# Kernel optimization log

Measured on AMD Instinct MI355X. Metric: run time of the kernel, lower is better.

The kernel has to match this reference:

```python
import jax, jax.numpy as jnp
import numpy as np

HEAD_NUM = 16
ROPE_BASE = 10000.0


def _rotate_half(x):
    # interleaved pairs: (x0,x1,x2,x3,...) -> (-x1,x0,-x3,x2,...)
    x_even = x[..., ::2]
    x_odd = x[..., 1::2]
    return jnp.stack((-x_odd, x_even), axis=-1).reshape(x.shape)


def _rope_cos_sin(seq_len, head_dim):
    half = head_dim // 2
    inv_freq = 1.0 / (ROPE_BASE ** (jnp.arange(half, dtype=jnp.float32) / half))
    t = jnp.arange(seq_len, dtype=jnp.float32)
    freqs = t[:, None] * inv_freq[None, :]            # [S, half]
    cos = jnp.repeat(jnp.cos(freqs), 2, axis=-1)       # [S, D]
    sin = jnp.repeat(jnp.sin(freqs), 2, axis=-1)       # [S, D]
    return cos, sin


def setup_inputs() -> dict:
    key = jax.random.key(0)
    ks = jax.random.split(key, 9)
    B, S, H = 2, 2048, 2048
    std = 1.0 / np.sqrt(H)
    return {
        "x": jax.random.normal(ks[0], (B, S, H), jnp.float32),
        "Wq": jax.random.normal(ks[1], (H, H), jnp.float32) * std,
        "bq": jax.random.normal(ks[2], (H,), jnp.float32) * std,
        "Wk": jax.random.normal(ks[3], (H, H), jnp.float32) * std,
        "bk": jax.random.normal(ks[4], (H,), jnp.float32) * std,
        "Wv": jax.random.normal(ks[5], (H, H), jnp.float32) * std,
        "bv": jax.random.normal(ks[6], (H,), jnp.float32) * std,
        "Wo": jax.random.normal(ks[7], (H, H), jnp.float32) * std,
        "bo": jax.random.normal(ks[8], (H,), jnp.float32) * std,
    }


def reference(x, Wq, bq, Wk, bk, Wv, bv, Wo, bo):
    B, S, H = x.shape
    nh = HEAD_NUM
    d = H // nh
    scale = jnp.float32(np.sqrt(d))

    def proj(W, b):
        y = x @ W.T + b                                 # torch Linear: x W^T + b
        return y.reshape(B, S, nh, d).transpose(0, 2, 1, 3)  # [B, nh, S, d]

    Q = proj(Wq, bq)
    K = proj(Wk, bk)
    V = proj(Wv, bv)

    cos, sin = _rope_cos_sin(S, d)                      # [S, d]
    Q = Q * cos + _rotate_half(Q) * sin
    K = K * cos + _rotate_half(K) * sin

    scores = jnp.einsum("bhqd,bhkd->bhqk", Q, K) / scale  # [B, nh, S, S]
    causal = jnp.tril(jnp.ones((S, S), dtype=bool))
    scores = jnp.where(causal, scores, jnp.float32(-jnp.inf))
    attn = jax.nn.softmax(scores, axis=-1)
    out = jnp.einsum("bhqk,bhkd->bhqd", attn, V)        # [B, nh, S, d]
    out = out.transpose(0, 2, 1, 3).reshape(B, S, H)
    return out @ Wo.T + bo
```

## Files before the change

### kernel.cpp

```cpp
#include <hip/hip_runtime.h>
#include <math.h>

typedef __bf16 bf16x8 __attribute__((ext_vector_type(8)));
typedef float floatx4 __attribute__((ext_vector_type(4)));

__device__ __forceinline__ unsigned short f32_to_bf16(float f) {
  unsigned int u = __float_as_uint(f);
  u = u + 0x7FFFu + ((u >> 16) & 1u);
  return (unsigned short)(u >> 16);
}
__device__ __forceinline__ float bf16_to_f32(unsigned short s) {
  return __uint_as_float(((unsigned int)s) << 16);
}

__device__ __forceinline__ void gld_lds16(const unsigned short* g,
                                          unsigned short* l) {
  __builtin_amdgcn_global_load_lds(
      (const __attribute__((address_space(1))) unsigned int*)g,
      (__attribute__((address_space(3))) unsigned int*)l, 16, 0, 0);
}

__global__ void cast_kernel(const float* __restrict__ in,
                            unsigned short* __restrict__ out, int n4) {
  int i = blockIdx.x * blockDim.x + threadIdx.x;
  if (i >= n4) return;
  const float4 v = reinterpret_cast<const float4*>(in)[i];
  ushort4 o;
  o.x = f32_to_bf16(v.x); o.y = f32_to_bf16(v.y);
  o.z = f32_to_bf16(v.z); o.w = f32_to_bf16(v.w);
  reinterpret_cast<ushort4*>(out)[i] = o;
}

__global__ void rope_table_kernel(float2* __restrict__ tab, int total) {
  int idx = blockIdx.x * blockDim.x + threadIdx.x;
  if (idx >= total) return;
  const int s = idx >> 6, i = idx & 63;
  const float inv = powf(10000.0f, -(float)i * (1.0f / 64.0f));
  const float ang = (float)s * inv;
  tab[idx] = make_float2(cosf(ang), sinf(ang));
}

template <int EPI>
__global__ __launch_bounds__(256) void gemm_fused(
    const unsigned short* __restrict__ A, const unsigned short* __restrict__ B,
    const float* __restrict__ bias, float* __restrict__ Cf,
    unsigned short* __restrict__ Cb, const float2* __restrict__ tab,
    float scl, int M, int N, int K, int S) {
  __shared__ unsigned short As[128 * 64];
  __shared__ unsigned short Bs[128 * 64];
  const int t = threadIdx.x;
  const int lane = t & 63;
  const int w = t >> 6;
  const int bm = blockIdx.y * 128;
  const int bn = blockIdx.x * 128;
  const int wm = (w & 1) * 64;
  const int wn = (w >> 1) * 64;
  const int m16 = lane & 15;
  const int quad = lane >> 4;
  const int key = m16 & 7;

  const int lr = lane >> 3;
  const int lc = ((lane & 7) ^ lr) * 8;

  floatx4 acc[4][4];
#pragma unroll
  for (int i = 0; i < 4; ++i)
#pragma unroll
    for (int j = 0; j < 4; ++j) acc[i][j] = floatx4{0.f, 0.f, 0.f, 0.f};

  const unsigned short* Abase = A + (size_t)(bm + w * 32 + lr) * K + lc;
  const unsigned short* Bbase = B + (size_t)(bn + w * 32 + lr) * K + lc;

  for (int k0 = 0; k0 < K; k0 += 64) {
    __syncthreads();
#pragma unroll
    for (int it = 0; it < 4; ++it) {
      gld_lds16(Abase + (size_t)it * 8 * K + k0, &As[(w * 4 + it) * 512]);
      gld_lds16(Bbase + (size_t)it * 8 * K + k0, &Bs[(w * 4 + it) * 512]);
    }
    __syncthreads();
#pragma unroll
    for (int ks = 0; ks < 64; ks += 32) {
      const int ck = ks >> 3;
      bf16x8 af[4], bfr[4];
#pragma unroll
      for (int i = 0; i < 4; ++i)
        af[i] = *reinterpret_cast<const bf16x8*>(
            &As[(wm + i * 16 + m16) * 64 + ((ck | quad) ^ key) * 8]);
#pragma unroll
      for (int j = 0; j < 4; ++j)
        bfr[j] = *reinterpret_cast<const bf16x8*>(
            &Bs[(wn + j * 16 + m16) * 64 + ((ck | quad) ^ key) * 8]);
#pragma unroll
      for (int i = 0; i < 4; ++i)
#pragma unroll
        for (int j = 0; j < 4; ++j)
          acc[i][j] = __builtin_amdgcn_mfma_f32_16x16x32_bf16(
              af[i], bfr[j], acc[i][j], 0, 0, 0);
    }
  }

#pragma unroll
  for (int i = 0; i < 4; ++i) {
    const int rbase = bm + wm + i * 16 + quad * 4;
#pragma unroll
    for (int j = 0; j < 4; ++j) {
      const int col = bn + wn + j * 16 + m16;
      const float bv = bias[col];
      if (EPI == 0) {
#pragma unroll
        for (int r = 0; r < 4; ++r)
          Cf[(size_t)(rbase + r) * N + col] = acc[i][j][r] + bv;
      } else if (EPI == 1) {
        const int pi = (col & 127) >> 1;
#pragma unroll
        for (int r = 0; r < 4; ++r) {
          const int row = rbase + r;
          const int s = row & (S - 1);
          const float v = acc[i][j][r] + bv;
          const float vp = __shfl_xor(v, 1);
          const float2 cs = tab[s * 64 + pi];
          const float oe = (v * cs.x - vp * cs.y) * scl;
          const float oo = (vp * cs.x + v * cs.y) * scl;
          if ((m16 & 1) == 0) {
            const unsigned pk =
                (unsigned)f32_to_bf16(oe) | ((unsigned)f32_to_bf16(oo) << 16);
            *reinterpret_cast<unsigned*>(Cb + (size_t)row * N + col) = pk;
          }
        }
      } else {
        const int b = rbase >> 11;
        const int s = rbase & (S - 1);
        ushort4 pk;
        pk.x = f32_to_bf16(acc[i][j][0] + bv);
        pk.y = f32_to_bf16(acc[i][j][1] + bv);
        pk.z = f32_to_bf16(acc[i][j][2] + bv);
        pk.w = f32_to_bf16(acc[i][j][3] + bv);
        *reinterpret_cast<ushort4*>(
            Cb + ((size_t)((b << 11) + col)) * S + s) = pk;
      }
    }
  }
}

constexpr int F_BQ = 128, F_BK = 64, F_DH = 128;
constexpr int KS_STR = 136;
constexpr int VS_STR = 72;
constexpr int PS_STR = 72;

__global__ __launch_bounds__(256, 2) void fattn_kernel(
    const unsigned short* __restrict__ Qb, const unsigned short* __restrict__ Kb,
    const unsigned short* __restrict__ Vtb, unsigned short* __restrict__ Ob,
    int S, int H, int nh) {
  __shared__ unsigned short Ks[F_BK * KS_STR];
  __shared__ unsigned short Vts[F_DH * VS_STR];
  __shared__ unsigned short Ps[F_BQ * PS_STR];

  const int t = threadIdx.x;
  const int lane = t & 63;
  const int w = t >> 6;
  const int l15 = lane & 15;
  const int quad = lane >> 4;

  const int i = blockIdx.x;
  const int bh = i & 31;
  const int qt = (i < 256) ? (i >> 5) : (15 - ((i - 256) >> 5));
  const int h = bh & 15;
  const int b = bh >> 4;
  const int q0 = qt * F_BQ;

  const unsigned short* Qrow = Qb + ((size_t)(b * S + q0)) * H + h * F_DH;
  const unsigned short* Krow = Kb + ((size_t)b * S) * H + h * F_DH;
  const unsigned short* Vtrow = Vtb + ((size_t)bh * F_DH) * S;
  unsigned short* Orow = Ob + ((size_t)(b * S + q0)) * H + h * F_DH;

  bf16x8 aq[2][4];
#pragma unroll
  for (int qg = 0; qg < 2; ++qg)
#pragma unroll
    for (int ks = 0; ks < 4; ++ks)
      aq[qg][ks] = *reinterpret_cast<const bf16x8*>(
          Qrow + (size_t)(w * 32 + qg * 16 + l15) * H + ks * 32 + quad * 8);

  floatx4 oacc[2][8];
#pragma unroll
  for (int qg = 0; qg < 2; ++qg)
#pragma unroll
    for (int dj = 0; dj < 8; ++dj) oacc[qg][dj] = floatx4{0.f, 0.f, 0.f, 0.f};
  float lpart[2][4] = {{0.f, 0.f, 0.f, 0.f}, {0.f, 0.f, 0.f, 0.f}};
  int qrow[2][4];
#pragma unroll
  for (int qg = 0; qg < 2; ++qg)
#pragma unroll
    for (int r = 0; r < 4; ++r)
      qrow[qg][r] = q0 + w * 32 + qg * 16 + quad * 4 + r;

  const int ntile = q0 / F_BK + 2;
  for (int tile = 0; tile < ntile; ++tile) {
    const int k0 = tile * F_BK;
    __syncthreads();
    {
      const int kt = t >> 2, c0 = (t & 3) * 32;
      const unsigned short* g = Krow + (size_t)(k0 + kt) * H + c0;
#pragma unroll
      for (int ii = 0; ii < 4; ++ii)
        *reinterpret_cast<uint4*>(&Ks[kt * KS_STR + c0 + ii * 8]) =
            *reinterpret_cast<const uint4*>(g + ii * 8);
    }
    {
      const int d = t >> 1, c0 = (t & 1) * 32;
      const unsigned short* g = Vtrow + (size_t)d * S + k0 + c0;
#pragma unroll
      for (int ii = 0; ii < 4; ++ii)
        *reinterpret_cast<uint4*>(&Vts[d * VS_STR + c0 + ii * 8]) =
            *reinterpret_cast<const uint4*>(g + ii * 8);
    }
    __syncthreads();

    floatx4 sacc[2][4];
#pragma unroll
    for (int qg = 0; qg < 2; ++qg)
#pragma unroll
      for (int j = 0; j < 4; ++j) sacc[qg][j] = floatx4{0.f, 0.f, 0.f, 0.f};
#pragma unroll
    for (int j = 0; j < 4; ++j) {
      bf16x8 bk[4];
#pragma unroll
      for (int ks = 0; ks < 4; ++ks)
        bk[ks] = *reinterpret_cast<const bf16x8*>(
            &Ks[(j * 16 + l15) * KS_STR + ks * 32 + quad * 8]);
#pragma unroll
      for (int qg = 0; qg < 2; ++qg)
#pragma unroll
        for (int ks = 0; ks < 4; ++ks)
          sacc[qg][j] = __builtin_amdgcn_mfma_f32_16x16x32_bf16(
              aq[qg][ks], bk[ks], sacc[qg][j], 0, 0, 0);
    }

#pragma unroll
    for (int qg = 0; qg < 2; ++qg)
#pragma unroll
      for (int j = 0; j < 4; ++j) {
        const int ktg = k0 + j * 16 + l15;
#pragma unroll
        for (int r = 0; r < 4; ++r) {
          const float p =
              (ktg <= qrow[qg][r]) ? exp2f(sacc[qg][j][r]) : 0.0f;
          lpart[qg][r] += p;
          Ps[(w * 32 + qg * 16 + quad * 4 + r) * PS_STR + j * 16 + l15] =
              f32_to_bf16(p);
        }
      }

#pragma unroll
    for (int ks2 = 0; ks2 < 2; ++ks2) {
      bf16x8 ap[2];
#pragma unroll
      for (int qg = 0; qg < 2; ++qg)
        ap[qg] = *reinterpret_cast<const bf16x8*>(
            &Ps[(w * 32 + qg * 16 + l15) * PS_STR + ks2 * 32 + quad * 8]);
#pragma unroll
      for (int dj = 0; dj < 8; ++dj) {
        const bf16x8 bv = *reinterpret_cast<const bf16x8*>(
            &Vts[(dj * 16 + l15) * VS_STR + ks2 * 32 + quad * 8]);
#pragma unroll
        for (int qg = 0; qg < 2; ++qg)
          oacc[qg][dj] = __builtin_amdgcn_mfma_f32_16x16x32_bf16(
              ap[qg], bv, oacc[qg][dj], 0, 0, 0);
      }
    }
  }

#pragma unroll
  for (int qg = 0; qg < 2; ++qg)
#pragma unroll
    for (int r = 0; r < 4; ++r) {
      float l = lpart[qg][r];
      l += __shfl_xor(l, 1);
      l += __shfl_xor(l, 2);
      l += __shfl_xor(l, 4);
      l += __shfl_xor(l, 8);
      const float linv = 1.0f / l;
      unsigned short* orow =
          Orow + (size_t)(w * 32 + qg * 16 + quad * 4 + r) * H;
#pragma unroll
      for (int dj = 0; dj < 8; ++dj)
        orow[dj * 16 + l15] = f32_to_bf16(oacc[qg][dj][r] * linv);
    }
}

extern "C" void kernel_launch(void* const* d_in, const int* in_sizes, int n_in,
                              void* d_out, int out_size, void* d_ws,
                              size_t ws_size, hipStream_t stream) {
  const float* x  = (const float*)d_in[0];
  const float* Wq = (const float*)d_in[1];
  const float* bq = (const float*)d_in[2];
  const float* Wk = (const float*)d_in[3];
  const float* bk = (const float*)d_in[4];
  const float* Wv = (const float*)d_in[5];
  const float* bv = (const float*)d_in[6];
  const float* Wo = (const float*)d_in[7];
  const float* bo = (const float*)d_in[8];
  float* out = (float*)d_out;

  const int B = 2, S = 2048, H = 2048, nh = 16;
  const int M = B * S;

  unsigned short* Wqb = (unsigned short*)d_ws;
  unsigned short* Wkb = Wqb + (size_t)H * H;
  unsigned short* Wvb = Wkb + (size_t)H * H;
  unsigned short* Wob = Wvb + (size_t)H * H;
  unsigned short* xb  = Wob + (size_t)H * H;
  unsigned short* Qbb = xb + (size_t)M * H;
  unsigned short* Kbb = Qbb + (size_t)M * H;
  unsigned short* Vtb = Kbb + (size_t)M * H;
  unsigned short* Ob  = Vtb + (size_t)M * H;
  float2* tab = (float2*)(Ob + (size_t)M * H);

  const int cast_w4 = H * H / 4;
  const int cast_x4 = M * H / 4;
  const int tab_n = S * 64;

  rope_table_kernel<<<dim3(tab_n / 256), dim3(256), 0, stream>>>(tab, tab_n);
  cast_kernel<<<dim3(cast_x4 / 256), dim3(256), 0, stream>>>(x, xb, cast_x4);
  cast_kernel<<<dim3(cast_w4 / 256), dim3(256), 0, stream>>>(Wq, Wqb, cast_w4);
  cast_kernel<<<dim3(cast_w4 / 256), dim3(256), 0, stream>>>(Wk, Wkb, cast_w4);
  cast_kernel<<<dim3(cast_w4 / 256), dim3(256), 0, stream>>>(Wv, Wvb, cast_w4);
  cast_kernel<<<dim3(cast_w4 / 256), dim3(256), 0, stream>>>(Wo, Wob, cast_w4);

  dim3 ggrid(H / 128, M / 128);
  const float qscale = 0.08838834764831845f * 1.4426950408889634f;

  gemm_fused<1><<<ggrid, dim3(256), 0, stream>>>(
      xb, Wqb, bq, nullptr, Qbb, tab, qscale, M, H, H, S);
  gemm_fused<1><<<ggrid, dim3(256), 0, stream>>>(
      xb, Wkb, bk, nullptr, Kbb, tab, 1.0f, M, H, H, S);
  gemm_fused<2><<<ggrid, dim3(256), 0, stream>>>(
      xb, Wvb, bv, nullptr, Vtb, nullptr, 1.0f, M, H, H, S);

  fattn_kernel<<<dim3((S / F_BQ) * B * nh), dim3(256), 0, stream>>>(
      Qbb, Kbb, Vtb, Ob, S, H, nh);

  gemm_fused<0><<<ggrid, dim3(256), 0, stream>>>(
      Ob, Wob, bo, out, nullptr, nullptr, 1.0f, M, H, H, S);
}
```

Before: 448.0 us.

## Fuse QKV projection into one GEMM and pre-swizzle K/V for direct LDS loads

Concatenates the Wq/Wk/Wv weights and biases so a single GEMM launch produces Q, K and V. The epilogue writes K in a per-head XOR-swizzled layout and V in a per-tile transposed, swizzled layout. The attention kernel can then stream K/V tiles into LDS with global_load_lds instead of register round-trips, using unpadded swizzled LDS buffers and 3 blocks per CU. It also packs P and output stores into 32-bit writes and reverses the q-tile scheduling order. This removes launch overhead and LDS padding and bank conflicts, at the cost of more complex index math and tighter register pressure.

```diff
diff --git a/kernel.cpp b/kernel.cpp
--- a/kernel.cpp
+++ b/kernel.cpp
@@ -8,9 +8,6 @@
   unsigned int u = __float_as_uint(f);
   u = u + 0x7FFFu + ((u >> 16) & 1u);
   return (unsigned short)(u >> 16);
-}
-__device__ __forceinline__ float bf16_to_f32(unsigned short s) {
-  return __uint_as_float(((unsigned int)s) << 16);
 }
 
 __device__ __forceinline__ void gld_lds16(const unsigned short* g,
@@ -31,6 +28,31 @@
   reinterpret_cast<ushort4*>(out)[i] = o;
 }
 
+__global__ void cast3_kernel(const float* __restrict__ w0,
+                             const float* __restrict__ w1,
+                             const float* __restrict__ w2,
+                             unsigned short* __restrict__ out, int n4each) {
+  int i = blockIdx.x * blockDim.x + threadIdx.x;
+  if (i >= 3 * n4each) return;
+  const int which = i / n4each;
+  const int off = i - which * n4each;
+  const float* src = (which == 0) ? w0 : (which == 1) ? w1 : w2;
+  const float4 v = reinterpret_cast<const float4*>(src)[off];
+  ushort4 o;
+  o.x = f32_to_bf16(v.x); o.y = f32_to_bf16(v.y);
+  o.z = f32_to_bf16(v.z); o.w = f32_to_bf16(v.w);
+  reinterpret_cast<ushort4*>(out)[i] = o;
+}
+
+__global__ void bcat_kernel(const float* __restrict__ bq,
+                            const float* __restrict__ bk,
+                            const float* __restrict__ bv,
+                            float* __restrict__ out) {
+  int i = blockIdx.x * blockDim.x + threadIdx.x;
+  const int which = i >> 11, off = i & 2047;
+  out[i] = (which == 0) ? bq[off] : (which == 1) ? bk[off] : bv[off];
+}
+
 __global__ void rope_table_kernel(float2* __restrict__ tab, int total) {
   int idx = blockIdx.x * blockDim.x + threadIdx.x;
   if (idx >= total) return;
@@ -44,8 +66,9 @@
 __global__ __launch_bounds__(256) void gemm_fused(
     const unsigned short* __restrict__ A, const unsigned short* __restrict__ B,
     const float* __restrict__ bias, float* __restrict__ Cf,
-    unsigned short* __restrict__ Cb, const float2* __restrict__ tab,
-    float scl, int M, int N, int K, int S) {
+    unsigned short* __restrict__ Qo, unsigned short* __restrict__ Ko,
+    unsigned short* __restrict__ Vo, const float2* __restrict__ tab,
+    float scl, int M, int N, int K) {
   __shared__ unsigned short As[128 * 64];
   __shared__ unsigned short Bs[128 * 64];
   const int t = threadIdx.x;
@@ -106,55 +129,68 @@
 #pragma unroll
     for (int j = 0; j < 4; ++j) {
       const int col = bn + wn + j * 16 + m16;
-      const float bv = bias[col];
+      const float bvv = bias[col];
       if (EPI == 0) {
 #pragma unroll
         for (int r = 0; r < 4; ++r)
-          Cf[(size_t)(rbase + r) * N + col] = acc[i][j][r] + bv;
-      } else if (EPI == 1) {
-        const int pi = (col & 127) >> 1;
-#pragma unroll
-        for (int r = 0; r < 4; ++r) {
-          const int row = rbase + r;
-          const int s = row & (S - 1);
-          const float v = acc[i][j][r] + bv;
-          const float vp = __shfl_xor(v, 1);
-          const float2 cs = tab[s * 64 + pi];
-          const float oe = (v * cs.x - vp * cs.y) * scl;
-          const float oo = (vp * cs.x + v * cs.y) * scl;
-          if ((m16 & 1) == 0) {
-            const unsigned pk =
-                (unsigned)f32_to_bf16(oe) | ((unsigned)f32_to_bf16(oo) << 16);
-            *reinterpret_cast<unsigned*>(Cb + (size_t)row * N + col) = pk;
+          Cf[(size_t)(rbase + r) * N + col] = acc[i][j][r] + bvv;
+      } else {
+        const int type = col >> 11;
+        const int vcol = col & 2047;
+        const int h = vcol >> 7, d = vcol & 127;
+        const int b = rbase >> 11;
+        if (type == 2) {
+          const int s0 = rbase & 2047;
+          const int kb = s0 >> 6, kse = s0 & 63;
+          const int c8 = ((kse >> 3) ^ (d & 7));
+          ushort4 pk;
+          pk.x = f32_to_bf16(acc[i][j][0] + bvv);
+          pk.y = f32_to_bf16(acc[i][j][1] + bvv);
+          pk.z = f32_to_bf16(acc[i][j][2] + bvv);
+          pk.w = f32_to_bf16(acc[i][j][3] + bvv);
+          *reinterpret_cast<ushort4*>(
+              Vo + (((size_t)(b * 16 + h) * 32 + kb) * 128 + d) * 64 +
+              c8 * 8 + (kse & 7)) = pk;
+        } else {
+          const float scl2 = (type == 0) ? scl : 1.0f;
+          const int pi = d >> 1;
+#pragma unroll
+          for (int r = 0; r < 4; ++r) {
+            const int row = rbase + r;
+            const int s = row & 2047;
+            const float v = acc[i][j][r] + bvv;
+            const float vp = __shfl_xor(v, 1);
+            const float2 cs = tab[s * 64 + pi];
+            const float oe = (v * cs.x - vp * cs.y) * scl2;
+            const float oo = (vp * cs.x + v * cs.y) * scl2;
+            if ((m16 & 1) == 0) {
+              const unsigned pk2 = (unsigned)f32_to_bf16(oe) |
+                                   ((unsigned)f32_to_bf16(oo) << 16);
+              if (type == 0) {
+                *reinterpret_cast<unsigned*>(Qo + (size_t)row * 2048 + vcol) =
+                    pk2;
+              } else {
+                const int dp = ((d >> 3) ^ (s & 15)) * 8 + (d & 7);
+                *reinterpret_cast<unsigned*>(
+                    Ko + ((size_t)(b * 16 + h) * 2048 + s) * 128 + dp) = pk2;
+              }
+            }
           }
         }
-      } else {
-        const int b = rbase >> 11;
-        const int s = rbase & (S - 1);
-        ushort4 pk;
-        pk.x = f32_to_bf16(acc[i][j][0] + bv);
-        pk.y = f32_to_bf16(acc[i][j][1] + bv);
-        pk.z = f32_to_bf16(acc[i][j][2] + bv);
-        pk.w = f32_to_bf16(acc[i][j][3] + bv);
-        *reinterpret_cast<ushort4*>(
-            Cb + ((size_t)((b << 11) + col)) * S + s) = pk;
       }
     }
   }
 }
 
 constexpr int F_BQ = 128, F_BK = 64, F_DH = 128;
-constexpr int KS_STR = 136;
-constexpr int VS_STR = 72;
-constexpr int PS_STR = 72;
-
-__global__ __launch_bounds__(256, 2) void fattn_kernel(
-    const unsigned short* __restrict__ Qb, const unsigned short* __restrict__ Kb,
-    const unsigned short* __restrict__ Vtb, unsigned short* __restrict__ Ob,
+
+__global__ __launch_bounds__(256, 3) void fattn_kernel(
+    const unsigned short* __restrict__ Qb, const unsigned short* __restrict__ Kh,
+    const unsigned short* __restrict__ Vt3, unsigned short* __restrict__ Ob,
     int S, int H, int nh) {
-  __shared__ unsigned short Ks[F_BK * KS_STR];
-  __shared__ unsigned short Vts[F_DH * VS_STR];
-  __shared__ unsigned short Ps[F_BQ * PS_STR];
+  __shared__ unsigned short Ks[64 * 128];
+  __shared__ unsigned short Vts[128 * 64];
+  __shared__ unsigned short Ps[128 * 64];
 
   const int t = threadIdx.x;
   const int lane = t & 63;
@@ -164,14 +200,14 @@
 
   const int i = blockIdx.x;
   const int bh = i & 31;
-  const int qt = (i < 256) ? (i >> 5) : (15 - ((i - 256) >> 5));
+  const int qt = (i < 256) ? (15 - (i >> 5)) : ((i - 256) >> 5);
   const int h = bh & 15;
   const int b = bh >> 4;
   const int q0 = qt * F_BQ;
 
   const unsigned short* Qrow = Qb + ((size_t)(b * S + q0)) * H + h * F_DH;
-  const unsigned short* Krow = Kb + ((size_t)b * S) * H + h * F_DH;
-  const unsigned short* Vtrow = Vtb + ((size_t)bh * F_DH) * S;
+  const unsigned short* Kbase = Kh + (size_t)bh * S * F_DH;
+  const unsigned short* Vbase = Vt3 + (size_t)bh * 32 * 8192;
   unsigned short* Orow = Ob + ((size_t)(b * S + q0)) * H + h * F_DH;
 
   bf16x8 aq[2][4];
@@ -194,26 +230,23 @@
 #pragma unroll
     for (int r = 0; r < 4; ++r)
       qrow[qg][r] = q0 + w * 32 + qg * 16 + quad * 4 + r;
+
+  const int lofs = lane * 8;
 
   const int ntile = q0 / F_BK + 2;
   for (int tile = 0; tile < ntile; ++tile) {
     const int k0 = tile * F_BK;
     __syncthreads();
     {
-      const int kt = t >> 2, c0 = (t & 3) * 32;
-      const unsigned short* g = Krow + (size_t)(k0 + kt) * H + c0;
-#pragma unroll
-      for (int ii = 0; ii < 4; ++ii)
-        *reinterpret_cast<uint4*>(&Ks[kt * KS_STR + c0 + ii * 8]) =
-            *reinterpret_cast<const uint4*>(g + ii * 8);
-    }
-    {
-      const int d = t >> 1, c0 = (t & 1) * 32;
-      const unsigned short* g = Vtrow + (size_t)d * S + k0 + c0;
-#pragma unroll
-      for (int ii = 0; ii < 4; ++ii)
-        *reinterpret_cast<uint4*>(&Vts[d * VS_STR + c0 + ii * 8]) =
-            *reinterpret_cast<const uint4*>(g + ii * 8);
+      const unsigned short* Ktile = Kbase + (size_t)k0 * 128;
+      const unsigned short* Vtile = Vbase + (size_t)(k0 >> 6) * 8192;
+#pragma unroll
+      for (int it = 0; it < 4; ++it) {
+        gld_lds16(Ktile + w * 2048 + it * 512 + lofs,
+                  &Ks[w * 2048 + it * 512]);
+        gld_lds16(Vtile + w * 2048 + it * 512 + lofs,
+                  &Vts[w * 2048 + it * 512]);
+      }
     }
     __syncthreads();
 
@@ -228,7 +261,7 @@
 #pragma unroll
       for (int ks = 0; ks < 4; ++ks)
         bk[ks] = *reinterpret_cast<const bf16x8*>(
-            &Ks[(j * 16 + l15) * KS_STR + ks * 32 + quad * 8]);
+            &Ks[(j * 16 + l15) * 128 + (((ks * 4 + quad) ^ l15) * 8)]);
 #pragma unroll
       for (int qg = 0; qg < 2; ++qg)
 #pragma unroll
@@ -242,13 +275,21 @@
 #pragma unroll
       for (int j = 0; j < 4; ++j) {
         const int ktg = k0 + j * 16 + l15;
+        const int cw = j * 2 + (l15 >> 3);
 #pragma unroll
         for (int r = 0; r < 4; ++r) {
           const float p =
               (ktg <= qrow[qg][r]) ? exp2f(sacc[qg][j][r]) : 0.0f;
           lpart[qg][r] += p;
-          Ps[(w * 32 + qg * 16 + quad * 4 + r) * PS_STR + j * 16 + l15] =
-              f32_to_bf16(p);
+          const float pp = __shfl_xor(p, 1);
+          if ((l15 & 1) == 0) {
+            const int prow = w * 32 + qg * 16 + quad * 4 + r;
+            const int cwp = cw ^ (prow & 7);
+            const unsigned pk = (unsigned)f32_to_bf16(p) |
+                                ((unsigned)f32_to_bf16(pp) << 16);
+            *reinterpret_cast<unsigned*>(
+                &Ps[prow * 64 + cwp * 8 + (l15 & 7)]) = pk;
+          }
         }
       }
 
@@ -258,11 +299,13 @@
 #pragma unroll
       for (int qg = 0; qg < 2; ++qg)
         ap[qg] = *reinterpret_cast<const bf16x8*>(
-            &Ps[(w * 32 + qg * 16 + l15) * PS_STR + ks2 * 32 + quad * 8]);
+            &Ps[(w * 32 + qg * 16 + l15) * 64 +
+                (((ks2 * 4 + quad) ^ (l15 & 7)) * 8)]);
 #pragma unroll
       for (int dj = 0; dj < 8; ++dj) {
         const bf16x8 bv = *reinterpret_cast<const bf16x8*>(
-            &Vts[(dj * 16 + l15) * VS_STR + ks2 * 32 + quad * 8]);
+            &Vts[(dj * 16 + l15) * 64 +
+                 (((ks2 * 4 + quad) ^ (l15 & 7)) * 8)]);
 #pragma unroll
         for (int qg = 0; qg < 2; ++qg)
           oacc[qg][dj] = __builtin_amdgcn_mfma_f32_16x16x32_bf16(
@@ -284,8 +327,15 @@
       unsigned short* orow =
           Orow + (size_t)(w * 32 + qg * 16 + quad * 4 + r) * H;
 #pragma unroll
-      for (int dj = 0; dj < 8; ++dj)
-        orow[dj * 16 + l15] = f32_to_bf16(oacc[qg][dj][r] * linv);
+      for (int dj = 0; dj < 8; ++dj) {
+        const float o = oacc[qg][dj][r] * linv;
+        const float op = __shfl_xor(o, 1);
+        if ((l15 & 1) == 0) {
+          const unsigned pk = (unsigned)f32_to_bf16(o) |
+                              ((unsigned)f32_to_bf16(op) << 16);
+          *reinterpret_cast<unsigned*>(orow + dj * 16 + l15) = pk;
+        }
+      }
     }
 }
 
@@ -306,41 +356,35 @@
   const int B = 2, S = 2048, H = 2048, nh = 16;
   const int M = B * S;
 
-  unsigned short* Wqb = (unsigned short*)d_ws;
-  unsigned short* Wkb = Wqb + (size_t)H * H;
-  unsigned short* Wvb = Wkb + (size_t)H * H;
-  unsigned short* Wob = Wvb + (size_t)H * H;
+  unsigned short* Wqkvb = (unsigned short*)d_ws;
+  unsigned short* Wob = Wqkvb + (size_t)3 * H * H;
   unsigned short* xb  = Wob + (size_t)H * H;
   unsigned short* Qbb = xb + (size_t)M * H;
-  unsigned short* Kbb = Qbb + (size_t)M * H;
-  unsigned short* Vtb = Kbb + (size_t)M * H;
-  unsigned short* Ob  = Vtb + (size_t)M * H;
-  float2* tab = (float2*)(Ob + (size_t)M * H);
+  unsigned short* Kh  = Qbb + (size_t)M * H;
+  unsigned short* Vt3 = Kh + (size_t)M * H;
+  unsigned short* Ob  = Vt3 + (size_t)M * H;
+  float* bqkv = (float*)(Ob + (size_t)M * H);
+  float2* tab = (float2*)(bqkv + 6144);
 
   const int cast_w4 = H * H / 4;
   const int cast_x4 = M * H / 4;
   const int tab_n = S * 64;
 
   rope_table_kernel<<<dim3(tab_n / 256), dim3(256), 0, stream>>>(tab, tab_n);
+  bcat_kernel<<<dim3(6144 / 256), dim3(256), 0, stream>>>(bq, bk, bv, bqkv);
+  cast3_kernel<<<dim3(3 * cast_w4 / 256), dim3(256), 0, stream>>>(
+      Wq, Wk, Wv, Wqkvb, cast_w4);
+  cast_kernel<<<dim3(cast_w4 / 256), dim3(256), 0, stream>>>(Wo, Wob, cast_w4);
   cast_kernel<<<dim3(cast_x4 / 256), dim3(256), 0, stream>>>(x, xb, cast_x4);
-  cast_kernel<<<dim3(cast_w4 / 256), dim3(256), 0, stream>>>(Wq, Wqb, cast_w4);
-  cast_kernel<<<dim3(cast_w4 / 256), dim3(256), 0, stream>>>(Wk, Wkb, cast_w4);
-  cast_kernel<<<dim3(cast_w4 / 256), dim3(256), 0, stream>>>(Wv, Wvb, cast_w4);
-  cast_kernel<<<dim3(cast_w4 / 256), dim3(256), 0, stream>>>(Wo, Wob, cast_w4);
-
-  dim3 ggrid(H / 128, M / 128);
+
   const float qscale = 0.08838834764831845f * 1.4426950408889634f;
 
-  gemm_fused<1><<<ggrid, dim3(256), 0, stream>>>(
-      xb, Wqb, bq, nullptr, Qbb, tab, qscale, M, H, H, S);
-  gemm_fused<1><<<ggrid, dim3(256), 0, stream>>>(
-      xb, Wkb, bk, nullptr, Kbb, tab, 1.0f, M, H, H, S);
-  gemm_fused<2><<<ggrid, dim3(256), 0, stream>>>(
-      xb, Wvb, bv, nullptr, Vtb, nullptr, 1.0f, M, H, H, S);
+  gemm_fused<1><<<dim3(3 * H / 128, M / 128), dim3(256), 0, stream>>>(
+      xb, Wqkvb, bqkv, nullptr, Qbb, Kh, Vt3, tab, qscale, M, 3 * H, H);
 
   fattn_kernel<<<dim3((S / F_BQ) * B * nh), dim3(256), 0, stream>>>(
-      Qbb, Kbb, Vtb, Ob, S, H, nh);
-
-  gemm_fused<0><<<ggrid, dim3(256), 0, stream>>>(
-      Ob, Wob, bo, out, nullptr, nullptr, 1.0f, M, H, H, S);
-}
+      Qbb, Kh, Vt3, Ob, S, H, nh);
+
+  gemm_fused<0><<<dim3(H / 128, M / 128), dim3(256), 0, stream>>>(
+      Ob, Wob, bo, out, nullptr, nullptr, nullptr, nullptr, 1.0f, M, H, H);
+}
```

Result: slower. 632.2 us (+41.1%).
